# Kernel tuning notes

Hardware: AMD Instinct MI355X
Metric: run time of the kernel (lower is better)

The kernel has to match this reference:

```python
import jax, jax.numpy as jnp
import numpy as np

NEG = -1e30  # finite stand-in for -inf so softmax grads stay clean


def setup_inputs() -> dict:
    key = jax.random.key(0)
    k1, k2 = jax.random.split(key)
    C, D = 8192, 512
    gt_class_embeddings = jax.random.normal(k1, (C, D), dtype=jnp.float32)
    w = jax.random.normal(k2, (C, D), dtype=jnp.float32)
    return {"gt_class_embeddings": gt_class_embeddings, "w": w}


def reference(gt_class_embeddings, w):
    # L2-normalize class embeddings, cosine-similarity matrix S (diag == 1)
    G = gt_class_embeddings / jnp.linalg.norm(gt_class_embeddings, axis=-1, keepdims=True)
    S = G @ G.T  # [C, C]
    C = S.shape[0]
    off_diag = ~jnp.eye(C, dtype=bool)

    # seSoftmax: per-row softmax over entries != 1 (off-diagonal); diagonal stays 1
    P = jax.nn.softmax(jnp.where(off_diag, S, NEG), axis=-1)
    S2 = jnp.where(off_diag, P, 1.0)

    # argsort(-S2)[1] == most similar (diag value 1 always ranks first),
    # argsort(-S2)[-1] == least similar == row min (softmax values < 1)
    ms = jnp.argmax(jnp.where(off_diag, S2, NEG), axis=-1)  # [C]
    ls = jnp.argmin(jnp.where(off_diag, S2, -NEG), axis=-1)  # [C]

    rows = jnp.arange(C)
    margin = S2[rows, ms] - S2[rows, ls]  # [C]

    d_ms = jnp.sqrt(jnp.sum((w - w[ms]) ** 2, axis=-1))  # [C]
    d_ls = jnp.sqrt(jnp.sum((w - w[ls]) ** 2, axis=-1))  # [C]

    loss = jnp.mean(jnp.maximum(0.0, d_ms - d_ls + margin))
    return loss
```

## Files before the change

### kernel.cpp

```cpp
#include <hip/hip_runtime.h>
#include <math.h>

#define CDIM 8192
#define DDIM 512
#define NEGF -3.0e38f
#define POSF  3.0e38f

#define BM 128
#define NSLOT (CDIM / BM)

typedef __attribute__((ext_vector_type(8))) short bf16x8;
typedef __attribute__((ext_vector_type(4))) float f32x4;

__device__ __forceinline__ unsigned short f2bf(float x) {
    unsigned int u = __float_as_uint(x);
    u += 0x7fffu + ((u >> 16) & 1u);
    return (unsigned short)(u >> 16);
}
__device__ __forceinline__ float bf2f(unsigned short h) {
    return __uint_as_float(((unsigned int)h) << 16);
}
__device__ __forceinline__ void gld16(const void* g, void* l) {
    __builtin_amdgcn_global_load_lds(
        (__attribute__((address_space(1))) void*)(void*)g,
        (__attribute__((address_space(3))) void*)l, 16, 0, 0);
}

__global__ __launch_bounds__(256) void k_prep(const float* __restrict__ g,
                                              unsigned short* __restrict__ hi,
                                              unsigned short* __restrict__ lo) {
    const int wave = threadIdx.x >> 6;
    const int lane = threadIdx.x & 63;
    const int row = blockIdx.x * 4 + wave;
    const float4* src = (const float4*)(g + (size_t)row * DDIM);
    const float4 a = src[lane * 2];
    const float4 b = src[lane * 2 + 1];
    float s = a.x * a.x + a.y * a.y + a.z * a.z + a.w * a.w +
              b.x * b.x + b.y * b.y + b.z * b.z + b.w * b.w;
#pragma unroll
    for (int m = 1; m < 64; m <<= 1) s += __shfl_xor(s, m, 64);
    const float rn = rsqrtf(s);
    const float y[8] = {a.x * rn, a.y * rn, a.z * rn, a.w * rn,
                        b.x * rn, b.y * rn, b.z * rn, b.w * rn};
    unsigned int hv[4], lv[4];
#pragma unroll
    for (int i = 0; i < 4; ++i) {
        const unsigned short h0 = f2bf(y[2 * i]);
        const unsigned short h1 = f2bf(y[2 * i + 1]);
        const unsigned short l0 = f2bf(y[2 * i] - bf2f(h0));
        const unsigned short l1 = f2bf(y[2 * i + 1] - bf2f(h1));
        hv[i] = (unsigned int)h0 | ((unsigned int)h1 << 16);
        lv[i] = (unsigned int)l0 | ((unsigned int)l1 << 16);
    }
    uint4* dh = (uint4*)(hi + (size_t)row * DDIM + lane * 8);
    uint4* dl = (uint4*)(lo + (size_t)row * DDIM + lane * 8);
    *dh = make_uint4(hv[0], hv[1], hv[2], hv[3]);
    *dl = make_uint4(lv[0], lv[1], lv[2], lv[3]);
}

__global__ __launch_bounds__(256, 2) void k_simstats(
    const unsigned short* __restrict__ ghi, const unsigned short* __restrict__ glo,
    float* __restrict__ pmax, float* __restrict__ pmin, float* __restrict__ pZ,
    int* __restrict__ pamax, int* __restrict__ pamin) {
    __shared__ unsigned short SH[4 * BM * 64];
    unsigned short* Ahi = SH;
    unsigned short* Alo = SH + 8192;
    unsigned short* Bhi = SH + 16384;
    unsigned short* Blo = SH + 24576;
    const int t = threadIdx.x;
    const int wave = t >> 6;
    const int lane = t & 63;
    const int lanelo = lane & 15;
    const int quad = lane >> 4;
    const int wr = wave & 1;
    const int wc = wave >> 1;

    const int bid = blockIdx.x;
    const int xcd = bid & 7;
    const int off = bid >> 3;
    int I, J, ntiles;
    if (off < 4) {
        const int d = xcd * 4 + off;
        I = 2 * d; J = I; ntiles = 2;
    } else {
        const int e = xcd * 252 + (off - 4);
        int Jf = (int)((1.0f + sqrtf(1.0f + 8.0f * (float)e)) * 0.5f);
        while ((Jf * (Jf - 1)) / 2 > e) --Jf;
        while (((Jf + 1) * Jf) / 2 <= e) ++Jf;
        J = Jf; I = e - (Jf * (Jf - 1)) / 2;
        ntiles = 1;
    }

    const int srow = t >> 3;
    const int scolb = ((t & 7) ^ ((t >> 3) & 7)) << 4;
    char* lAh = (char*)Ahi + t * 16;
    char* lAl = (char*)Alo + t * 16;
    char* lBh = (char*)Bhi + t * 16;
    char* lBl = (char*)Blo + t * 16;

    float* rm  = (float*)SH;
    float* rz  = rm + 256;
    float* rmn = rz + 256;
    int*   ra  = (int*)(rmn + 256);
    int*   ran = ra + 256;
    float* cm  = (float*)Bhi;
    float* cz  = cm + 256;
    float* cmn = cz + 256;
    int*   ca  = (int*)(cmn + 256);
    int*   can = ca + 256;

    const int l7 = lanelo & 7;

    for (int tl = 0; tl < ntiles; ++tl) {
        const int Ie = I + tl, Je = J + tl;
        const int i0 = Ie * BM;
        const int j0 = Je * BM;
        const bool isdiag = (Ie == Je);

        f32x4 acc[4][4];
#pragma unroll
        for (int rt = 0; rt < 4; ++rt)
#pragma unroll
            for (int ct = 0; ct < 4; ++ct)
                acc[rt][ct] = (f32x4){0.f, 0.f, 0.f, 0.f};

        const char* baseAh = (const char*)ghi + (size_t)(i0 + srow) * 1024 + scolb;
        const char* baseAl = (const char*)glo + (size_t)(i0 + srow) * 1024 + scolb;
        const char* baseBh = (const char*)ghi + (size_t)(j0 + srow) * 1024 + scolb;
        const char* baseBl = (const char*)glo + (size_t)(j0 + srow) * 1024 + scolb;

        for (int k0 = 0; k0 < DDIM; k0 += 64) {
            __syncthreads();
#pragma unroll
            for (int q = 0; q < 4; ++q) {
                const size_t roff = (size_t)q * 32 * 1024 + k0 * 2;
                gld16(baseAh + roff, lAh + q * 4096);
                gld16(baseAl + roff, lAl + q * 4096);
                gld16(baseBh + roff, lBh + q * 4096);
                gld16(baseBl + roff, lBl + q * 4096);
            }
            __syncthreads();
#pragma unroll
            for (int ks = 0; ks < 2; ++ks) {
                const int sl8 = ((((ks << 2) + quad) ^ l7) << 3);
                bf16x8 ah[4], al[4];
#pragma unroll
                for (int rt = 0; rt < 4; ++rt) {
                    const int ro = ((wr * 64 + rt * 16 + lanelo) << 6) + sl8;
                    ah[rt] = *(const bf16x8*)&Ahi[ro];
                    al[rt] = *(const bf16x8*)&Alo[ro];
                }
#pragma unroll
                for (int ct = 0; ct < 4; ++ct) {
                    const int co = ((wc * 64 + ct * 16 + lanelo) << 6) + sl8;
                    const bf16x8 bh = *(const bf16x8*)&Bhi[co];
                    const bf16x8 bl = *(const bf16x8*)&Blo[co];
#pragma unroll
                    for (int rt = 0; rt < 4; ++rt) {
                        acc[rt][ct] = __builtin_amdgcn_mfma_f32_16x16x32_bf16(
                            ah[rt], bh, acc[rt][ct], 0, 0, 0);
                        acc[rt][ct] = __builtin_amdgcn_mfma_f32_16x16x32_bf16(
                            ah[rt], bl, acc[rt][ct], 0, 0, 0);
                        acc[rt][ct] = __builtin_amdgcn_mfma_f32_16x16x32_bf16(
                            al[rt], bh, acc[rt][ct], 0, 0, 0);
                    }
                }
            }
        }

        __syncthreads();

#pragma unroll
        for (int rt = 0; rt < 4; ++rt) {
#pragma unroll
            for (int r = 0; r < 4; ++r) {
                const int lrow = wr * 64 + rt * 16 + quad * 4 + r;
                const int gi = i0 + lrow;
                float tmax = NEGF; int targ = 0x7fffffff;
                float tmin = POSF; int targn = 0x7fffffff;
                float vv[4];
#pragma unroll
                for (int ct = 0; ct < 4; ++ct) {
                    const int gj = j0 + wc * 64 + ct * 16 + lanelo;
                    const float v = acc[rt][ct][r];
                    const bool dg = isdiag && (gj == gi);
                    const float vM = dg ? NEGF : v;
                    const float vm = dg ? POSF : v;
                    vv[ct] = vM;
                    if (vM > tmax) { tmax = vM; targ = gj; }
                    if (vm < tmin) { tmin = vm; targn = gj; }
                }
                float se = 0.f;
#pragma unroll
                for (int ct = 0; ct < 4; ++ct) se += __expf(vv[ct] - tmax);
                float vmax = tmax; int imax = targ;
                float vmin = tmin; int imin = targn;
#pragma unroll
                for (int msk = 1; msk < 16; msk <<= 1) {
                    const float v2 = __shfl_xor(vmax, msk, 64);
                    const int i2 = __shfl_xor(imax, msk, 64);
                    if (v2 > vmax || (v2 == vmax && i2 < imax)) { vmax = v2; imax = i2; }
                    const float v3 = __shfl_xor(vmin, msk, 64);
                    const int i3 = __shfl_xor(imin, msk, 64);
                    if (v3 < vmin || (v3 == vmin && i3 < imin)) { vmin = v3; imin = i3; }
                }
                float zs = se * __expf(tmax - vmax);
#pragma unroll
                for (int msk = 1; msk < 16; msk <<= 1) zs += __shfl_xor(zs, msk, 64);
                if (lanelo == 0) {
                    const int o = wc * 128 + lrow;
                    rm[o] = vmax; rz[o] = zs; rmn[o] = vmin;
                    ra[o] = imax; ran[o] = imin;
                }
            }
        }

        if (!isdiag) {
#pragma unroll
            for (int ct = 0; ct < 4; ++ct) {
                const int lcol = wc * 64 + ct * 16 + lanelo;
                float tmax = NEGF; int targ = 0x7fffffff;
                float tmin = POSF; int targn = 0x7fffffff;
#pragma unroll
                for (int rt = 0; rt < 4; ++rt)
#pragma unroll
                    for (int r = 0; r < 4; ++r) {
                        const int gi = i0 + wr * 64 + rt * 16 + quad * 4 + r;
                        const float v = acc[rt][ct][r];
                        if (v > tmax) { tmax = v; targ = gi; }
                        if (v < tmin) { tmin = v; targn = gi; }
                    }
                float se = 0.f;
#pragma unroll
                for (int rt = 0; rt < 4; ++rt)
#pragma unroll
                    for (int r = 0; r < 4; ++r)
                        se += __expf(acc[rt][ct][r] - tmax);
#pragma unroll
                for (int msk = 16; msk < 64; msk <<= 1) {
                    const float m2 = __shfl_xor(tmax, msk, 64);
                    const int i2 = __shfl_xor(targ, msk, 64);
                    const float z2 = __shfl_xor(se, msk, 64);
                    const float mn2 = __shfl_xor(tmin, msk, 64);
                    const int in2 = __shfl_xor(targn, msk, 64);
                    const float M = fmaxf(tmax, m2);
                    se = se * __expf(tmax - M) + z2 * __expf(m2 - M);
                    if (m2 > tmax || (m2 == tmax && i2 < targ)) { targ = i2; }
                    tmax = M;
                    if (mn2 < tmin || (mn2 == tmin && in2 < targn)) { tmin = mn2; targn = in2; }
                }
                if (quad == 0) {
                    const int o = wr * 128 + lcol;
                    cm[o] = tmax; cz[o] = se; cmn[o] = tmin;
                    ca[o] = targ; can[o] = targn;
                }
            }
        }

        __syncthreads();

        if (t < BM) {
            const float m0 = rm[t], m1 = rm[128 + t];
            float vmax = m0; int imax = ra[t];
            if (m1 > vmax) { vmax = m1; imax = ra[128 + t]; }
            float vmin = rmn[t]; int imin = ran[t];
            if (rmn[128 + t] < vmin) { vmin = rmn[128 + t]; imin = ran[128 + t]; }
            const float zs = rz[t] * __expf(m0 - vmax) +
                             rz[128 + t] * __expf(m1 - vmax);
            const size_t o = (size_t)Je * CDIM + i0 + t;
            pmax[o] = vmax; pmin[o] = vmin; pZ[o] = zs;
            pamax[o] = imax; pamin[o] = imin;
        } else if (!isdiag) {
            const int tt = t - BM;
            const float m0 = cm[tt], m1 = cm[128 + tt];
            float vmax = m0; int imax = ca[tt];
            if (m1 > vmax) { vmax = m1; imax = ca[128 + tt]; }
            float vmin = cmn[tt]; int imin = can[tt];
            if (cmn[128 + tt] < vmin) { vmin = cmn[128 + tt]; imin = can[128 + tt]; }
            const float zs = cz[tt] * __expf(m0 - vmax) +
                             cz[128 + tt] * __expf(m1 - vmax);
            const size_t o = (size_t)Ie * CDIM + j0 + tt;
            pmax[o] = vmax; pmin[o] = vmin; pZ[o] = zs;
            pamax[o] = imax; pamin[o] = imin;
        }
    }
}

__global__ __launch_bounds__(256) void k_lossc(
    const float* __restrict__ pmax, const float* __restrict__ pmin,
    const float* __restrict__ pZ, const int* __restrict__ pamax,
    const int* __restrict__ pamin, const float* __restrict__ w,
    float* __restrict__ vals) {
    const int wave = threadIdx.x >> 6;
    const int lane = threadIdx.x & 63;
    const int row = blockIdx.x * 4 + wave;
    const size_t o = (size_t)lane * CDIM + row;
    const float m0 = pmax[o];
    float v = m0; int a = pamax[o];
    float u = pmin[o]; int b = pamin[o];
#pragma unroll
    for (int msk = 1; msk < 64; msk <<= 1) {
        const float v2 = __shfl_xor(v, msk, 64);
        const int i2 = __shfl_xor(a, msk, 64);
        if (v2 > v || (v2 == v && i2 < a)) { v = v2; a = i2; }
        const float v3 = __shfl_xor(u, msk, 64);
        const int i3 = __shfl_xor(b, msk, 64);
        if (v3 < u || (v3 == u && i3 < b)) { u = v3; b = i3; }
    }
    float z = pZ[o] * __expf(m0 - v);
#pragma unroll
    for (int msk = 1; msk < 64; msk <<= 1) z += __shfl_xor(z, msk, 64);
    const float margin = (1.f - __expf(u - v)) / z;
    const int jm = a, jl = b;

    const float4* wi = (const float4*)(w + (size_t)row * DDIM);
    const float4* wm = (const float4*)(w + (size_t)jm * DDIM);
    const float4* wl = (const float4*)(w + (size_t)jl * DDIM);
    float sm = 0.f, sl = 0.f;
#pragma unroll
    for (int h = 0; h < 2; ++h) {
        const int idx = h * 64 + lane;
        const float4 x = wi[idx];
        const float4 y = wm[idx];
        const float4 c = wl[idx];
        float d;
        d = x.x - y.x; sm = fmaf(d, d, sm);
        d = x.y - y.y; sm = fmaf(d, d, sm);
        d = x.z - y.z; sm = fmaf(d, d, sm);
        d = x.w - y.w; sm = fmaf(d, d, sm);
        d = x.x - c.x; sl = fmaf(d, d, sl);
        d = x.y - c.y; sl = fmaf(d, d, sl);
        d = x.z - c.z; sl = fmaf(d, d, sl);
        d = x.w - c.w; sl = fmaf(d, d, sl);
    }
#pragma unroll
    for (int msk = 1; msk < 64; msk <<= 1) {
        sm += __shfl_xor(sm, msk, 64);
        sl += __shfl_xor(sl, msk, 64);
    }
    if (lane == 0) {
        const float val = sqrtf(sm) - sqrtf(sl) + margin;
        vals[row] = val > 0.f ? val : 0.f;
    }
}

__global__ __launch_bounds__(256) void k_final(const float* __restrict__ vals,
                                               float* __restrict__ out) {
    __shared__ float red[256];
    float s = 0.f;
    for (int i = threadIdx.x; i < CDIM; i += 256) s += vals[i];
    red[threadIdx.x] = s;
    __syncthreads();
#pragma unroll
    for (int k = 128; k > 0; k >>= 1) {
        if (threadIdx.x < (unsigned)k) red[threadIdx.x] += red[threadIdx.x + k];
        __syncthreads();
    }
    if (threadIdx.x == 0) out[0] = red[0] * (1.0f / CDIM);
}

extern "C" void kernel_launch(void* const* d_in, const int* in_sizes, int n_in,
                              void* d_out, int out_size, void* d_ws, size_t ws_size,
                              hipStream_t stream) {
    const float* g = (const float*)d_in[0];
    const float* w = (const float*)d_in[1];
    float* out = (float*)d_out;

    unsigned short* ghi = (unsigned short*)d_ws;
    unsigned short* glo = ghi + (size_t)CDIM * DDIM;
    float* p = (float*)(glo + (size_t)CDIM * DDIM);
    float* pmax = p;      p += (size_t)NSLOT * CDIM;
    float* pmin = p;      p += (size_t)NSLOT * CDIM;
    float* pZ = p;        p += (size_t)NSLOT * CDIM;
    int* pamax = (int*)p; p += (size_t)NSLOT * CDIM;
    int* pamin = (int*)p; p += (size_t)NSLOT * CDIM;
    float* vals = p;      p += CDIM;

    k_prep<<<CDIM / 4, 256, 0, stream>>>(g, ghi, glo);
    k_simstats<<<2048, 256, 0, stream>>>(ghi, glo, pmax, pmin, pZ, pamax, pamin);
    k_lossc<<<CDIM / 4, 256, 0, stream>>>(pmax, pmin, pZ, pamax, pamin, w, vals);
    k_final<<<1, 256, 0, stream>>>(vals, out);
}
```

Before: 276.6 us.

## Use fixed softmax shift of one, halve K tile, raise occupancy

The softmax partition sum is now taken with a fixed shift of 1, which is safe because cosine similarities are bounded by 1. This removes the running-max rescaling and the extra shuffles of the online max merge in the stats kernel and the final reduction. The K tile of the similarity GEMM is halved to 32 with a new LDS swizzle, which shrinks shared memory so launch bounds can ask for 3 blocks per SM. The trade-off is twice as many barrier-separated load steps per tile and higher register pressure at 3 waves.

```diff
diff --git a/kernel.cpp b/kernel.cpp
--- a/kernel.cpp
+++ b/kernel.cpp
@@ -58,15 +58,15 @@
     *dl = make_uint4(lv[0], lv[1], lv[2], lv[3]);
 }
 
-__global__ __launch_bounds__(256, 2) void k_simstats(
+__global__ __launch_bounds__(256, 3) void k_simstats(
     const unsigned short* __restrict__ ghi, const unsigned short* __restrict__ glo,
     float* __restrict__ pmax, float* __restrict__ pmin, float* __restrict__ pZ,
     int* __restrict__ pamax, int* __restrict__ pamin) {
-    __shared__ unsigned short SH[4 * BM * 64];
+    __shared__ unsigned short SH[4 * BM * 32];
     unsigned short* Ahi = SH;
-    unsigned short* Alo = SH + 8192;
-    unsigned short* Bhi = SH + 16384;
-    unsigned short* Blo = SH + 24576;
+    unsigned short* Alo = SH + 4096;
+    unsigned short* Bhi = SH + 8192;
+    unsigned short* Blo = SH + 12288;
     const int t = threadIdx.x;
     const int wave = t >> 6;
     const int lane = t & 63;
@@ -91,12 +91,16 @@
         ntiles = 1;
     }
 
-    const int srow = t >> 3;
-    const int scolb = ((t & 7) ^ ((t >> 3) & 7)) << 4;
+    const int srow = t >> 2;
+    const int scolb = ((t & 3) ^ ((t >> 3) & 3)) << 4;
     char* lAh = (char*)Ahi + t * 16;
     char* lAl = (char*)Alo + t * 16;
     char* lBh = (char*)Bhi + t * 16;
     char* lBl = (char*)Blo + t * 16;
+
+    const int fsl = (quad ^ ((lanelo >> 1) & 3)) << 3;
+    const int aoff = (wr * 64 + lanelo) * 32 + fsl;
+    const int boff = (wc * 64 + lanelo) * 32 + fsl;
 
     float* rm  = (float*)SH;
     float* rz  = rm + 256;
@@ -109,8 +113,6 @@
     int*   ca  = (int*)(cmn + 256);
     int*   can = ca + 256;
 
-    const int l7 = lanelo & 7;
-
     for (int tl = 0; tl < ntiles; ++tl) {
         const int Ie = I + tl, Je = J + tl;
         const int i0 = Ie * BM;
@@ -129,41 +131,35 @@
         const char* baseBh = (const char*)ghi + (size_t)(j0 + srow) * 1024 + scolb;
         const char* baseBl = (const char*)glo + (size_t)(j0 + srow) * 1024 + scolb;
 
-        for (int k0 = 0; k0 < DDIM; k0 += 64) {
+        for (int k0 = 0; k0 < DDIM; k0 += 32) {
             __syncthreads();
 #pragma unroll
-            for (int q = 0; q < 4; ++q) {
-                const size_t roff = (size_t)q * 32 * 1024 + k0 * 2;
+            for (int q = 0; q < 2; ++q) {
+                const size_t roff = (size_t)q * 64 * 1024 + k0 * 2;
                 gld16(baseAh + roff, lAh + q * 4096);
                 gld16(baseAl + roff, lAl + q * 4096);
                 gld16(baseBh + roff, lBh + q * 4096);
                 gld16(baseBl + roff, lBl + q * 4096);
             }
             __syncthreads();
-#pragma unroll
-            for (int ks = 0; ks < 2; ++ks) {
-                const int sl8 = ((((ks << 2) + quad) ^ l7) << 3);
-                bf16x8 ah[4], al[4];
+            bf16x8 ah[4], al[4];
+#pragma unroll
+            for (int rt = 0; rt < 4; ++rt) {
+                ah[rt] = *(const bf16x8*)&Ahi[aoff + rt * 512];
+                al[rt] = *(const bf16x8*)&Alo[aoff + rt * 512];
+            }
+#pragma unroll
+            for (int ct = 0; ct < 4; ++ct) {
+                const bf16x8 bh = *(const bf16x8*)&Bhi[boff + ct * 512];
+                const bf16x8 bl = *(const bf16x8*)&Blo[boff + ct * 512];
 #pragma unroll
                 for (int rt = 0; rt < 4; ++rt) {
-                    const int ro = ((wr * 64 + rt * 16 + lanelo) << 6) + sl8;
-                    ah[rt] = *(const bf16x8*)&Ahi[ro];
-                    al[rt] = *(const bf16x8*)&Alo[ro];
-                }
-#pragma unroll
-                for (int ct = 0; ct < 4; ++ct) {
-                    const int co = ((wc * 64 + ct * 16 + lanelo) << 6) + sl8;
-                    const bf16x8 bh = *(const bf16x8*)&Bhi[co];
-                    const bf16x8 bl = *(const bf16x8*)&Blo[co];
-#pragma unroll
-                    for (int rt = 0; rt < 4; ++rt) {
-                        acc[rt][ct] = __builtin_amdgcn_mfma_f32_16x16x32_bf16(
-                            ah[rt], bh, acc[rt][ct], 0, 0, 0);
-                        acc[rt][ct] = __builtin_amdgcn_mfma_f32_16x16x32_bf16(
-                            ah[rt], bl, acc[rt][ct], 0, 0, 0);
-                        acc[rt][ct] = __builtin_amdgcn_mfma_f32_16x16x32_bf16(
-                            al[rt], bh, acc[rt][ct], 0, 0, 0);
-                    }
+                    acc[rt][ct] = __builtin_amdgcn_mfma_f32_16x16x32_bf16(
+                        ah[rt], bh, acc[rt][ct], 0, 0, 0);
+                    acc[rt][ct] = __builtin_amdgcn_mfma_f32_16x16x32_bf16(
+                        ah[rt], bl, acc[rt][ct], 0, 0, 0);
+                    acc[rt][ct] = __builtin_amdgcn_mfma_f32_16x16x32_bf16(
+                        al[rt], bh, acc[rt][ct], 0, 0, 0);
                 }
             }
         }
@@ -178,7 +174,6 @@
                 const int gi = i0 + lrow;
                 float tmax = NEGF; int targ = 0x7fffffff;
                 float tmin = POSF; int targn = 0x7fffffff;
-                float vv[4];
 #pragma unroll
                 for (int ct = 0; ct < 4; ++ct) {
                     const int gj = j0 + wc * 64 + ct * 16 + lanelo;
@@ -186,31 +181,22 @@
                     const bool dg = isdiag && (gj == gi);
                     const float vM = dg ? NEGF : v;
                     const float vm = dg ? POSF : v;
-                    vv[ct] = vM;
                     if (vM > tmax) { tmax = vM; targ = gj; }
                     if (vm < tmin) { tmin = vm; targn = gj; }
                 }
-                float se = 0.f;
-#pragma unroll
-                for (int ct = 0; ct < 4; ++ct) se += __expf(vv[ct] - tmax);
-                float vmax = tmax; int imax = targ;
-                float vmin = tmin; int imin = targn;
 #pragma unroll
                 for (int msk = 1; msk < 16; msk <<= 1) {
-                    const float v2 = __shfl_xor(vmax, msk, 64);
-                    const int i2 = __shfl_xor(imax, msk, 64);
-                    if (v2 > vmax || (v2 == vmax && i2 < imax)) { vmax = v2; imax = i2; }
-                    const float v3 = __shfl_xor(vmin, msk, 64);
-                    const int i3 = __shfl_xor(imin, msk, 64);
-                    if (v3 < vmin || (v3 == vmin && i3 < imin)) { vmin = v3; imin = i3; }
-                }
-                float zs = se * __expf(tmax - vmax);
-#pragma unroll
-                for (int msk = 1; msk < 16; msk <<= 1) zs += __shfl_xor(zs, msk, 64);
+                    const float v2 = __shfl_xor(tmax, msk, 64);
+                    const int i2 = __shfl_xor(targ, msk, 64);
+                    if (v2 > tmax || (v2 == tmax && i2 < targ)) { tmax = v2; targ = i2; }
+                    const float v3 = __shfl_xor(tmin, msk, 64);
+                    const int i3 = __shfl_xor(targn, msk, 64);
+                    if (v3 < tmin || (v3 == tmin && i3 < targn)) { tmin = v3; targn = i3; }
+                }
                 if (lanelo == 0) {
                     const int o = wc * 128 + lrow;
-                    rm[o] = vmax; rz[o] = zs; rmn[o] = vmin;
-                    ra[o] = imax; ran[o] = imin;
+                    rm[o] = tmax; rmn[o] = tmin;
+                    ra[o] = targ; ran[o] = targn;
                 }
             }
         }
@@ -230,30 +216,62 @@
                         if (v > tmax) { tmax = v; targ = gi; }
                         if (v < tmin) { tmin = v; targn = gi; }
                     }
-                float se = 0.f;
-#pragma unroll
-                for (int rt = 0; rt < 4; ++rt)
-#pragma unroll
-                    for (int r = 0; r < 4; ++r)
-                        se += __expf(acc[rt][ct][r] - tmax);
 #pragma unroll
                 for (int msk = 16; msk < 64; msk <<= 1) {
                     const float m2 = __shfl_xor(tmax, msk, 64);
                     const int i2 = __shfl_xor(targ, msk, 64);
-                    const float z2 = __shfl_xor(se, msk, 64);
+                    if (m2 > tmax || (m2 == tmax && i2 < targ)) { tmax = m2; targ = i2; }
                     const float mn2 = __shfl_xor(tmin, msk, 64);
                     const int in2 = __shfl_xor(targn, msk, 64);
-                    const float M = fmaxf(tmax, m2);
-                    se = se * __expf(tmax - M) + z2 * __expf(m2 - M);
-                    if (m2 > tmax || (m2 == tmax && i2 < targ)) { targ = i2; }
-                    tmax = M;
                     if (mn2 < tmin || (mn2 == tmin && in2 < targn)) { tmin = mn2; targn = in2; }
                 }
                 if (quad == 0) {
                     const int o = wr * 128 + lcol;
-                    cm[o] = tmax; cz[o] = se; cmn[o] = tmin;
+                    cm[o] = tmax; cmn[o] = tmin;
                     ca[o] = targ; can[o] = targn;
                 }
+            }
+        }
+
+#pragma unroll
+        for (int rt = 0; rt < 4; ++rt)
+#pragma unroll
+            for (int ct = 0; ct < 4; ++ct)
+#pragma unroll
+                for (int r = 0; r < 4; ++r) {
+                    float e = __expf(acc[rt][ct][r] - 1.f);
+                    if (isdiag) {
+                        const int gi = i0 + wr * 64 + rt * 16 + quad * 4 + r;
+                        const int gj = j0 + wc * 64 + ct * 16 + lanelo;
+                        if (gi == gj) e = 0.f;
+                    }
+                    acc[rt][ct][r] = e;
+                }
+
+#pragma unroll
+        for (int rt = 0; rt < 4; ++rt)
+#pragma unroll
+            for (int r = 0; r < 4; ++r) {
+                float s = acc[rt][0][r] + acc[rt][1][r] +
+                          acc[rt][2][r] + acc[rt][3][r];
+#pragma unroll
+                for (int msk = 1; msk < 16; msk <<= 1) s += __shfl_xor(s, msk, 64);
+                if (lanelo == 0)
+                    rz[wc * 128 + wr * 64 + rt * 16 + quad * 4 + r] = s;
+            }
+
+        if (!isdiag) {
+#pragma unroll
+            for (int ct = 0; ct < 4; ++ct) {
+                float s = 0.f;
+#pragma unroll
+                for (int rt = 0; rt < 4; ++rt)
+                    s += acc[rt][ct][0] + acc[rt][ct][1] +
+                         acc[rt][ct][2] + acc[rt][ct][3];
+#pragma unroll
+                for (int msk = 16; msk < 64; msk <<= 1) s += __shfl_xor(s, msk, 64);
+                if (quad == 0)
+                    cz[wr * 128 + wc * 64 + ct * 16 + lanelo] = s;
             }
         }
 
@@ -265,10 +283,8 @@
             if (m1 > vmax) { vmax = m1; imax = ra[128 + t]; }
             float vmin = rmn[t]; int imin = ran[t];
             if (rmn[128 + t] < vmin) { vmin = rmn[128 + t]; imin = ran[128 + t]; }
-            const float zs = rz[t] * __expf(m0 - vmax) +
-                             rz[128 + t] * __expf(m1 - vmax);
             const size_t o = (size_t)Je * CDIM + i0 + t;
-            pmax[o] = vmax; pmin[o] = vmin; pZ[o] = zs;
+            pmax[o] = vmax; pmin[o] = vmin; pZ[o] = rz[t] + rz[128 + t];
             pamax[o] = imax; pamin[o] = imin;
         } else if (!isdiag) {
             const int tt = t - BM;
@@ -277,10 +293,8 @@
             if (m1 > vmax) { vmax = m1; imax = ca[128 + tt]; }
             float vmin = cmn[tt]; int imin = can[tt];
             if (cmn[128 + tt] < vmin) { vmin = cmn[128 + tt]; imin = can[128 + tt]; }
-            const float zs = cz[tt] * __expf(m0 - vmax) +
-                             cz[128 + tt] * __expf(m1 - vmax);
             const size_t o = (size_t)Ie * CDIM + j0 + tt;
-            pmax[o] = vmax; pmin[o] = vmin; pZ[o] = zs;
+            pmax[o] = vmax; pmin[o] = vmin; pZ[o] = cz[tt] + cz[128 + tt];
             pamax[o] = imax; pamin[o] = imin;
         }
     }
@@ -295,9 +309,9 @@
     const int lane = threadIdx.x & 63;
     const int row = blockIdx.x * 4 + wave;
     const size_t o = (size_t)lane * CDIM + row;
-    const float m0 = pmax[o];
-    float v = m0; int a = pamax[o];
+    float v = pmax[o]; int a = pamax[o];
     float u = pmin[o]; int b = pamin[o];
+    float z = pZ[o];
 #pragma unroll
     for (int msk = 1; msk < 64; msk <<= 1) {
         const float v2 = __shfl_xor(v, msk, 64);
@@ -306,11 +320,9 @@
         const float v3 = __shfl_xor(u, msk, 64);
         const int i3 = __shfl_xor(b, msk, 64);
         if (v3 < u || (v3 == u && i3 < b)) { u = v3; b = i3; }
-    }
-    float z = pZ[o] * __expf(m0 - v);
-#pragma unroll
-    for (int msk = 1; msk < 64; msk <<= 1) z += __shfl_xor(z, msk, 64);
-    const float margin = (1.f - __expf(u - v)) / z;
+        z += __shfl_xor(z, msk, 64);
+    }
+    const float margin = (1.f - __expf(u - v)) * __expf(v - 1.f) / z;
     const int jm = a, jl = b;
 
     const float4* wi = (const float4*)(w + (size_t)row * DDIM);
```

Result: faster. 253.9 us (-8.2%).
